# Kernel tuning notes

Measured on AMD Instinct MI355X. Metric: run time of the kernel, lower is better.

Reference implementation:

```python
import jax, jax.numpy as jnp
import numpy as np

B, L, E, H, K = 128, 512, 512, 256, 64


def setup_inputs() -> dict:
    key = jax.random.key(0)
    ks = jax.random.split(key, 13)
    s = 1.0 / np.sqrt(H)

    def u(k, shape):
        return jax.random.uniform(k, shape, jnp.float32, -s, s)

    return {
        "input_batch": jax.random.normal(ks[0], (B, L, E), jnp.float32),
        "labels": jax.random.randint(ks[1], (B, L), 0, K),
        "w_ih_f": u(ks[2], (4 * H, E)),
        "w_hh_f": u(ks[3], (4 * H, H)),
        "b_ih_f": u(ks[4], (4 * H,)),
        "b_hh_f": u(ks[5], (4 * H,)),
        "w_ih_b": u(ks[6], (4 * H, E)),
        "w_hh_b": u(ks[7], (4 * H, H)),
        "b_ih_b": u(ks[8], (4 * H,)),
        "b_hh_b": u(ks[9], (4 * H,)),
        "w_emit": u(ks[10], (K, 2 * H)),
        "b_emit": jnp.zeros((K,), jnp.float32),
        "transition": jax.random.normal(ks[11], (K, K), jnp.float32),
    }


def _lstm_dir(x, w_ih, w_hh, b_ih, b_hh):
    """One LSTM direction. x: (L,B,E) -> hidden states (L,B,H). PyTorch gate order i,f,g,o."""
    Hh = w_hh.shape[1]
    # input contribution for all timesteps at once: (L,B,4H)
    pre = jnp.einsum('lbe,ge->lbg', x, w_ih) + b_ih + b_hh

    def step(carry, p_t):
        h, c = carry
        g = p_t + h @ w_hh.T  # (B,4H)
        i, f, gg, o = jnp.split(g, 4, axis=-1)
        c = jax.nn.sigmoid(f) * c + jax.nn.sigmoid(i) * jnp.tanh(gg)
        h = jax.nn.sigmoid(o) * jnp.tanh(c)
        return (h, c), h

    init = (jnp.zeros((x.shape[1], Hh), x.dtype), jnp.zeros((x.shape[1], Hh), x.dtype))
    _, hs = jax.lax.scan(step, init, pre)
    return hs


def _bilstm_crf_loss(input_batch, labels, w_ih_f, w_hh_f, b_ih_f, b_hh_f,
                     w_ih_b, w_hh_b, b_ih_b, b_hh_b, w_emit, b_emit, transition):
    x = jnp.transpose(input_batch, (1, 0, 2))  # (L,B,E)
    h_f = _lstm_dir(x, w_ih_f, w_hh_f, b_ih_f, b_hh_f)
    h_b = _lstm_dir(x[::-1], w_ih_b, w_hh_b, b_ih_b, b_hh_b)[::-1]
    h = jnp.concatenate([h_f, h_b], axis=-1)  # (L,B,2H)
    emit = jnp.einsum('lbh,kh->b018'.replace('018', 'lk'), h, w_emit) + b_emit  # placeholder fixed below
    emit = jnp.einsum('lbh,kh->lbk', h, w_emit) + b_emit  # (L,B,K)
    emit = jnp.transpose(emit, (1, 0, 2))  # (B,L,K)

    # gold path score
    gold_emit = jnp.take_along_axis(emit, labels[:, :, None], axis=2)[:, :, 0]  # (B,L)
    gold_trans = transition[labels[:, :-1], labels[:, 1:]]  # (B,L-1)
    total_score = gold_emit.sum(axis=1) + gold_trans.sum(axis=1)  # (B,)

    # CRF forward algorithm (log partition), scan over timesteps 1..L-1
    def crf_step(d, e_t):
        # d: (B,K) log alpha; e_t: (B,K) emit at step t
        d = jax.nn.logsumexp(d[:, :, None] + transition[None, :, :] + e_t[:, None, :], axis=1)
        return d, None

    d0 = emit[:, 0]  # (B,K)
    dT, _ = jax.lax.scan(crf_step, d0, jnp.transpose(emit[:, 1:], (1, 0, 2)))
    log_z = jax.nn.logsumexp(dT, axis=1)  # (B,)
    return -(total_score - log_z)  # (B,)


def reference(input_batch, labels, w_ih_f, w_hh_f, b_ih_f, b_hh_f,
              w_ih_b, w_hh_b, b_ih_b, b_hh_b, w_emit, b_emit, transition):
    return _bilstm_crf_loss(input_batch, labels, w_ih_f, w_hh_f, b_ih_f, b_hh_f,
                            w_ih_b, w_hh_b, b_ih_b, b_hh_b, w_emit, b_emit, transition)
```

## Files before the change

### kernel.cpp

```cpp
#include <hip/hip_runtime.h>
#include <hip/hip_bf16.h>

#define B_   128
#define L_   512
#define E_   512
#define H_   256
#define K_   64
#define G4H  1024
#define LOG2E 1.4426950408889634f

typedef __bf16 bf16x8 __attribute__((ext_vector_type(8)));
typedef float  f32x4  __attribute__((ext_vector_type(4)));
typedef int    i32x8  __attribute__((ext_vector_type(8)));

__device__ inline unsigned short f2bf(float f) {
    unsigned int x = __builtin_bit_cast(unsigned int, f);
    unsigned int r = (x + 0x7fffu + ((x >> 16) & 1u)) >> 16;
    return (unsigned short)r;
}
__device__ inline float bf2f(unsigned short u) {
    unsigned int x = ((unsigned int)u) << 16;
    return __builtin_bit_cast(float, x);
}
__device__ inline unsigned int pack2(float lo, float hi) {
    return (unsigned int)f2bf(lo) | ((unsigned int)f2bf(hi) << 16);
}
__device__ inline float ex2(float x) { return __builtin_amdgcn_exp2f(x); }
__device__ inline float rcp_(float x) { return __builtin_amdgcn_rcpf(x); }

__device__ inline void gl_lds16(const unsigned short* g, unsigned short* l) {
    __builtin_amdgcn_global_load_lds(
        (const __attribute__((address_space(1))) unsigned int*)g,
        (__attribute__((address_space(3))) unsigned int*)l, 16, 0, 0);
}

__global__ void setup_convert(const float* __restrict__ whh_f, const float* __restrict__ whh_b,
                              const float* __restrict__ wemit,
                              const float* __restrict__ wihf, const float* __restrict__ wihb,
                              const float* __restrict__ bihf, const float* __restrict__ bhhf,
                              const float* __restrict__ bihb, const float* __restrict__ bhhb,
                              unsigned char* __restrict__ whh8,
                              unsigned short* __restrict__ wemit_bf,
                              unsigned short* __restrict__ wp,
                              float* __restrict__ bias_p) {
    int i = blockIdx.x * 256 + threadIdx.x;
    if (i < 262144) {
        int j = 2 * i;
        float v0 = (j < 262144) ? whh_f[j] : whh_b[j - 262144];
        float v1 = (j + 1 < 262144) ? whh_f[j + 1] : whh_b[j + 1 - 262144];
        int pk = __builtin_amdgcn_cvt_pk_fp8_f32(v0 * LOG2E, v1 * LOG2E, 0, false);
        ((unsigned short*)whh8)[i] = (unsigned short)(pk & 0xffff);
    }
    if (i < K_ * 2 * H_) wemit_bf[i] = f2bf(wemit[i]);
    if (i < 131072) {
        int rp = i >> 6;
        int k8 = (i & 63) * 8;
        int dd = rp >> 10, np = rp & 1023;
        int srow = (np & 3) * 256 + (np >> 2);
        const float* src = (dd == 0 ? wihf : wihb) + (size_t)srow * 512 + k8;
        float4 a  = *reinterpret_cast<const float4*>(src);
        float4 b2 = *reinterpret_cast<const float4*>(src + 4);
        uint4 pk = { pack2(a.x * LOG2E, a.y * LOG2E), pack2(a.z * LOG2E, a.w * LOG2E),
                     pack2(b2.x * LOG2E, b2.y * LOG2E), pack2(b2.z * LOG2E, b2.w * LOG2E) };
        *reinterpret_cast<uint4*>(wp + (size_t)rp * 512 + k8) = pk;
    }
    if (i < 2048) {
        int dd = i >> 10, np = i & 1023;
        int srow = (np & 3) * 256 + (np >> 2);
        bias_p[i] = ((dd == 0) ? (bihf[srow] + bhhf[srow]) : (bihb[srow] + bhhb[srow])) * LOG2E;
    }
}

__global__ void convert_x(const float* __restrict__ x, unsigned short* __restrict__ xb) {
    int i = blockIdx.x * 256 + threadIdx.x;
    float4 a = reinterpret_cast<const float4*>(x)[i * 2];
    float4 b = reinterpret_cast<const float4*>(x)[i * 2 + 1];
    uint4 p = { pack2(a.x, a.y), pack2(a.z, a.w), pack2(b.x, b.y), pack2(b.z, b.w) };
    reinterpret_cast<uint4*>(xb)[i] = p;
}

__global__ __launch_bounds__(256) void pre_gemm(
    const unsigned short* __restrict__ xb,
    const unsigned short* __restrict__ wp,
    const float* __restrict__ bias_p,
    unsigned short* __restrict__ pre3)
{
    __shared__ unsigned short A_lds[128 * 32];
    __shared__ unsigned short B_lds[128 * 32];

    int nt = blockIdx.x, mt = blockIdx.y;
    int tid = threadIdx.x;
    int n0 = nt * 128;
    int b  = mt >> 2, l0 = (mt & 3) * 128;
    int w = tid >> 6, lane = tid & 63;
    int q = lane >> 4, ln = lane & 15;
    int wm = (w >> 1) * 64, wn = (w & 1) * 64;

    f32x4 acc[4][4];
    #pragma unroll
    for (int i = 0; i < 4; ++i)
        #pragma unroll
        for (int j = 0; j < 4; ++j) acc[i][j] = (f32x4){0.f, 0.f, 0.f, 0.f};

    int r_ = tid >> 2, kp = (tid & 3) * 8;
    const unsigned short* asrc0 = xb + ((size_t)b * 512 + l0 + r_) * 512 + kp;
    const unsigned short* asrc1 = asrc0 + (size_t)64 * 512;
    const unsigned short* bsrc0 = wp + (size_t)(n0 + r_) * 512 + kp;
    const unsigned short* bsrc1 = bsrc0 + (size_t)64 * 512;
    unsigned short* adst0 = &A_lds[tid * 8];
    unsigned short* adst1 = &A_lds[2048 + tid * 8];
    unsigned short* bdst0 = &B_lds[tid * 8];
    unsigned short* bdst1 = &B_lds[2048 + tid * 8];

    for (int kc = 0; kc < 16; ++kc) {
        int k0 = kc * 32;
        gl_lds16(asrc0 + k0, adst0);
        gl_lds16(asrc1 + k0, adst1);
        gl_lds16(bsrc0 + k0, bdst0);
        gl_lds16(bsrc1 + k0, bdst1);
        __syncthreads();

        bf16x8 af[4], bfv[4];
        #pragma unroll
        for (int ms = 0; ms < 4; ++ms)
            af[ms] = *reinterpret_cast<const bf16x8*>(&A_lds[(wm + ms * 16 + ln) * 32 + q * 8]);
        #pragma unroll
        for (int ns = 0; ns < 4; ++ns)
            bfv[ns] = *reinterpret_cast<const bf16x8*>(&B_lds[(wn + ns * 16 + ln) * 32 + q * 8]);
        #pragma unroll
        for (int ms = 0; ms < 4; ++ms)
            #pragma unroll
            for (int ns = 0; ns < 4; ++ns)
                acc[ms][ns] = __builtin_amdgcn_mfma_f32_16x16x32_bf16(af[ms], bfv[ns], acc[ms][ns], 0, 0, 0);
        __syncthreads();
    }

    #pragma unroll
    for (int ns = 0; ns < 4; ++ns) {
        int n = n0 + wn + ns * 16 + ln;
        float bias = bias_p[n];
        int dsel = n >> 10, np = n & 1023;
        #pragma unroll
        for (int ms = 0; ms < 4; ++ms) {
            #pragma unroll
            for (int rg = 0; rg < 4; ++rg) {
                int l = l0 + wm + ms * 16 + q * 4 + rg;
                pre3[(((size_t)dsel * 128 + b) * 512 + l) * 1024 + np] = f2bf(acc[ms][ns][rg] + bias);
            }
        }
    }
}

__global__ __launch_bounds__(512, 2) void lstm_scan(
    const unsigned short* __restrict__ pre3,
    const unsigned char* __restrict__ whh8,
    unsigned short* __restrict__ hcat)
{
    __shared__ unsigned char h_lds[2][256];

    int wg = blockIdx.x;
    int d = wg >> 7, b = wg & 127;
    int tid = threadIdx.x, w = tid >> 6, lane = tid & 63;
    int q = lane >> 4, ln = lane & 15;

    const unsigned char* whh_d = whh8 + (size_t)d * (1024 * 256);
    const unsigned short* pre_wg = pre3 + ((size_t)d * 128 + b) * (512 * 1024);

    i32x8 wh[4][2][2];
    #pragma unroll
    for (int g = 0; g < 4; ++g)
        #pragma unroll
        for (int s = 0; s < 2; ++s) {
            int row = g * 256 + (w + 8 * s) * 16 + ln;
            #pragma unroll
            for (int kc = 0; kc < 2; ++kc)
                wh[g][s][kc] = *reinterpret_cast<const i32x8*>(
                    whh_d + (size_t)row * 256 + kc * 128 + q * 32);
        }

    if (tid < 128) ((int*)h_lds)[tid] = 0;

    bool act = (lane < 32);
    int s_  = (lane >> 4) & 1;
    int col = (w + 8 * s_) * 16 + ln;

    ushort4 p0 = {0,0,0,0}, p1 = {0,0,0,0};
    if (act) {
        int la  = (d == 0) ? 0 : (L_ - 1);
        int lb_ = (d == 0) ? 1 : (L_ - 2);
        p0 = *reinterpret_cast<const ushort4*>(pre_wg + (size_t)la * 1024 + col * 4);
        p1 = *reinterpret_cast<const ushort4*>(pre_wg + (size_t)lb_ * 1024 + col * 4);
    }
    __syncthreads();

    float cst = 0.f;

    for (int t = 0; t < L_; ++t) {
        int p = t & 1;
        int l = (d == 0) ? t : (L_ - 1 - t);

        ushort4 p2 = {0,0,0,0};
        if (act) {
            int t2 = (t + 2 < L_) ? (t + 2) : (L_ - 1);
            int l2 = (d == 0) ? t2 : (L_ - 1 - t2);
            p2 = *reinterpret_cast<const ushort4*>(pre_wg + (size_t)l2 * 1024 + col * 4);
        }

        const unsigned char* hb = h_lds[p];
        uint4 a00 = *reinterpret_cast<const uint4*>(hb + q * 32);
        uint4 a01 = *reinterpret_cast<const uint4*>(hb + q * 32 + 16);
        uint4 a10 = *reinterpret_cast<const uint4*>(hb + 128 + q * 32);
        uint4 a11 = *reinterpret_cast<const uint4*>(hb + 128 + q * 32 + 16);
        i32x8 af0 = { (int)a00.x, (int)a00.y, (int)a00.z, (int)a00.w,
                      (int)a01.x, (int)a01.y, (int)a01.z, (int)a01.w };
        i32x8 af1 = { (int)a10.x, (int)a10.y, (int)a10.z, (int)a10.w,
                      (int)a11.x, (int)a11.y, (int)a11.z, (int)a11.w };

        f32x4 acc[4][2];
        #pragma unroll
        for (int g = 0; g < 4; ++g) {
            acc[g][0] = (f32x4){0.f, 0.f, 0.f, 0.f};
            acc[g][1] = (f32x4){0.f, 0.f, 0.f, 0.f};
        }
        #pragma unroll
        for (int g = 0; g < 4; ++g)
            acc[g][0] = __builtin_amdgcn_mfma_scale_f32_16x16x128_f8f6f4(
                af0, wh[g][0][0], acc[g][0], 0, 0, 0, 0x7f7f7f7f, 0, 0x7f7f7f7f);
        #pragma unroll
        for (int g = 0; g < 4; ++g)
            acc[g][0] = __builtin_amdgcn_mfma_scale_f32_16x16x128_f8f6f4(
                af1, wh[g][0][1], acc[g][0], 0, 0, 0, 0x7f7f7f7f, 0, 0x7f7f7f7f);
        float lo[4];
        #pragma unroll
        for (int g = 0; g < 4; ++g) lo[g] = __shfl(acc[g][0][0], ln);
        __builtin_amdgcn_sched_barrier(0);
        #pragma unroll
        for (int g = 0; g < 4; ++g)
            acc[g][1] = __builtin_amdgcn_mfma_scale_f32_16x16x128_f8f6f4(
                af0, wh[g][1][0], acc[g][1], 0, 0, 0, 0x7f7f7f7f, 0, 0x7f7f7f7f);
        #pragma unroll
        for (int g = 0; g < 4; ++g)
            acc[g][1] = __builtin_amdgcn_mfma_scale_f32_16x16x128_f8f6f4(
                af1, wh[g][1][1], acc[g][1], 0, 0, 0, 0x7f7f7f7f, 0, 0x7f7f7f7f);
        float hi[4];
        #pragma unroll
        for (int g = 0; g < 4; ++g) hi[g] = __shfl(acc[g][1][0], ln);

        if (act) {
            float vi = (s_ ? hi[0] : lo[0]) + bf2f(p0.x);
            float vf = (s_ ? hi[1] : lo[1]) + bf2f(p0.y);
            float vg = (s_ ? hi[2] : lo[2]) + bf2f(p0.z);
            float vo = (s_ ? hi[3] : lo[3]) + bf2f(p0.w);
            float ei  = ex2(vi);
            float e2g = ex2(vg + vg);
            float itg = (ei * (e2g - 1.f)) * rcp_((1.f + ei) * (1.f + e2g));
            float sf  = rcp_(1.f + ex2(-vf));
            float cn  = fmaf(sf, cst, itg);
            cst = cn;
            float tc  = fmaf(-2.f, rcp_(1.f + ex2((2.f * LOG2E) * cn)), 1.f);
            float so  = rcp_(1.f + ex2(-vo));
            float hn  = so * tc;
            int pk = __builtin_amdgcn_cvt_pk_fp8_f32(hn, hn, 0, false);
            h_lds[p ^ 1][col] = (unsigned char)(pk & 0xff);
            hcat[((size_t)l * 128 + b) * 512 + d * 256 + col] = f2bf(hn);
        }
        __syncthreads();

        p0 = p1; p1 = p2;
    }
}

__global__ __launch_bounds__(256) void emit_gemm(
    const unsigned short* __restrict__ hcat,
    const unsigned short* __restrict__ wemit,
    const float* __restrict__ bemit,
    float* __restrict__ emit)
{
    int m0 = blockIdx.x * 64;
    int tid = threadIdx.x, w = tid >> 6, lane = tid & 63;
    int quad = lane >> 4, ln = lane & 15;
    int mrow = m0 + w * 16;

    f32x4 acc[4];
    #pragma unroll
    for (int i = 0; i < 4; ++i) acc[i] = (f32x4){0.f, 0.f, 0.f, 0.f};

    const unsigned short* arow = hcat + (size_t)(mrow + ln) * 512;
    #pragma unroll 4
    for (int kc = 0; kc < 16; ++kc) {
        bf16x8 af = *reinterpret_cast<const bf16x8*>(arow + kc * 32 + quad * 8);
        #pragma unroll
        for (int T = 0; T < 4; ++T) {
            bf16x8 bfv = *reinterpret_cast<const bf16x8*>(wemit + (size_t)(T * 16 + ln) * 512 + kc * 32 + quad * 8);
            acc[T] = __builtin_amdgcn_mfma_f32_16x16x32_bf16(af, bfv, acc[T], 0, 0, 0);
        }
    }
    #pragma unroll
    for (int T = 0; T < 4; ++T) {
        int k = T * 16 + ln;
        float bias = bemit[k];
        #pragma unroll
        for (int rg = 0; rg < 4; ++rg) {
            int m = mrow + quad * 4 + rg;
            int ll = m >> 7, bidx = m & 127;
            emit[((size_t)bidx * L_ + ll) * K_ + k] = acc[T][rg] + bias;
        }
    }
}

__global__ __launch_bounds__(64) void crf_kernel(
    const float* __restrict__ emit,
    const int* __restrict__ labels,
    const float* __restrict__ trans,
    float* __restrict__ out)
{
    __shared__ float els[2][64];
    int b = blockIdx.x, lane = threadIdx.x;
    const float* eb = emit + (size_t)b * L_ * K_;
    const int* lb = labels + (size_t)b * L_;

    float gold = 0.f;
    for (int t = lane; t < L_; t += 64) gold += eb[(size_t)t * K_ + lb[t]];
    for (int t = lane; t < L_ - 1; t += 64) gold += trans[lb[t] * K_ + lb[t + 1]];
    #pragma unroll
    for (int off = 32; off; off >>= 1) gold += __shfl_down(gold, off);

    float expT[64];
    #pragma unroll
    for (int i = 0; i < 64; ++i) expT[i] = __expf(trans[i * K_ + lane]);

    float dstate = eb[lane];
    float enext = eb[K_ + lane];
    for (int t = 1; t < L_; ++t) {
        float ecur = enext;
        if (t + 1 < L_) enext = eb[(size_t)(t + 1) * K_ + lane];
        float M = __builtin_amdgcn_readfirstlane(dstate);
        float e = __expf(dstate - M);
        float* el = els[t & 1];
        el[lane] = e;
        asm volatile("s_waitcnt lgkmcnt(0)" ::: "memory");
        float s0 = 0.f, s1 = 0.f, s2 = 0.f, s3 = 0.f;
        #pragma unroll
        for (int i = 0; i < 64; i += 16) {
            float4 a0 = *reinterpret_cast<const float4*>(&el[i]);
            float4 a1 = *reinterpret_cast<const float4*>(&el[i + 4]);
            float4 a2 = *reinterpret_cast<const float4*>(&el[i + 8]);
            float4 a3 = *reinterpret_cast<const float4*>(&el[i + 12]);
            s0 = fmaf(a0.x, expT[i], s0);      s0 = fmaf(a0.y, expT[i + 1], s0);
            s0 = fmaf(a0.z, expT[i + 2], s0);  s0 = fmaf(a0.w, expT[i + 3], s0);
            s1 = fmaf(a1.x, expT[i + 4], s1);  s1 = fmaf(a1.y, expT[i + 5], s1);
            s1 = fmaf(a1.z, expT[i + 6], s1);  s1 = fmaf(a1.w, expT[i + 7], s1);
            s2 = fmaf(a2.x, expT[i + 8], s2);  s2 = fmaf(a2.y, expT[i + 9], s2);
            s2 = fmaf(a2.z, expT[i + 10], s2); s2 = fmaf(a2.w, expT[i + 11], s2);
            s3 = fmaf(a3.x, expT[i + 12], s3); s3 = fmaf(a3.y, expT[i + 13], s3);
            s3 = fmaf(a3.z, expT[i + 14], s3); s3 = fmaf(a3.w, expT[i + 15], s3);
        }
        dstate = M + __logf((s0 + s1) + (s2 + s3)) + ecur;
    }
    float M = __builtin_amdgcn_readfirstlane(dstate);
    float e = __expf(dstate - M);
    float s = e;
    #pragma unroll
    for (int off = 32; off; off >>= 1) s += __shfl_xor(s, off);
    float logZ = M + __logf(s);
    if (lane == 0) out[b] = -(gold - logZ);
}

#define OFF_PRE    ((size_t)0)
#define OFF_EMIT   OFF_PRE
#define OFF_HCAT   ((size_t)268435456)
#define OFF_XB     OFF_HCAT
#define OFF_WHH8   ((size_t)(OFF_HCAT + 67108864))
#define OFF_WEMIT  ((size_t)(OFF_WHH8 + 524288))
#define OFF_WP     ((size_t)(OFF_WEMIT + 65536))
#define OFF_BIAS   ((size_t)(OFF_WP + 2097152))

extern "C" void kernel_launch(void* const* d_in, const int* in_sizes, int n_in,
                              void* d_out, int out_size, void* d_ws, size_t ws_size,
                              hipStream_t stream) {
    const float* x      = (const float*)d_in[0];
    const int*   labels = (const int*)d_in[1];
    const float* wihf   = (const float*)d_in[2];
    const float* whhf   = (const float*)d_in[3];
    const float* bihf   = (const float*)d_in[4];
    const float* bhhf   = (const float*)d_in[5];
    const float* wihb   = (const float*)d_in[6];
    const float* whhb   = (const float*)d_in[7];
    const float* bihb   = (const float*)d_in[8];
    const float* bhhb   = (const float*)d_in[9];
    const float* wemit  = (const float*)d_in[10];
    const float* bemit  = (const float*)d_in[11];
    const float* trans  = (const float*)d_in[12];
    float* out = (float*)d_out;

    char* ws = (char*)d_ws;
    unsigned short* pre3   = (unsigned short*)(ws + OFF_PRE);
    unsigned short* hcat   = (unsigned short*)(ws + OFF_HCAT);
    unsigned short* xb     = (unsigned short*)(ws + OFF_XB);
    float*          emit   = (float*)(ws + OFF_EMIT);
    unsigned char*  whh8   = (unsigned char*)(ws + OFF_WHH8);
    unsigned short* we_bf  = (unsigned short*)(ws + OFF_WEMIT);
    unsigned short* wp     = (unsigned short*)(ws + OFF_WP);
    float*          bias_p = (float*)(ws + OFF_BIAS);

    setup_convert<<<1024, 256, 0, stream>>>(whhf, whhb, wemit, wihf, wihb,
                                            bihf, bhhf, bihb, bhhb,
                                            whh8, we_bf, wp, bias_p);
    convert_x<<<16384, 256, 0, stream>>>(x, xb);
    pre_gemm<<<dim3(16, 512), 256, 0, stream>>>(xb, wp, bias_p, pre3);
    lstm_scan<<<256, 512, 0, stream>>>(pre3, whh8, hcat);
    emit_gemm<<<1024, 256, 0, stream>>>(hcat, we_bf, bemit, emit);
    crf_kernel<<<128, 64, 0, stream>>>(emit, labels, trans, out);
}
```

Baseline: 1.107 ms.

## Skew LSTM recurrence halves across two barriers to overlap MFMA with gate math

Splits each recurrent timestep into two phases, each closed by a barrier. Lanes handling the lower half of the hidden columns finish their gates in phase two of step t. Lanes handling the upper half finish theirs for step t-1 in phase one of step t, while the first-half K-chunk MFMAs are issuing. This software-pipelines the dependency chain so gate math overlaps matrix work. In exchange it adds a second barrier per step, a prologue and epilogue, and more complex indexing that must keep the h buffers consistent.

```diff
diff --git a/kernel.cpp b/kernel.cpp
--- a/kernel.cpp
+++ b/kernel.cpp
@@ -186,71 +186,49 @@
 
     ushort4 p0 = {0,0,0,0}, p1 = {0,0,0,0};
     if (act) {
-        int la  = (d == 0) ? 0 : (L_ - 1);
-        int lb_ = (d == 0) ? 1 : (L_ - 2);
-        p0 = *reinterpret_cast<const ushort4*>(pre_wg + (size_t)la * 1024 + col * 4);
-        p1 = *reinterpret_cast<const ushort4*>(pre_wg + (size_t)lb_ * 1024 + col * 4);
+        int ta = 0;
+        int tb = 1 - s_;
+        int la  = (d == 0) ? ta : (L_ - 1 - ta);
+        int lb2 = (d == 0) ? tb : (L_ - 1 - tb);
+        p0 = *reinterpret_cast<const ushort4*>(pre_wg + (size_t)la  * 1024 + col * 4);
+        p1 = *reinterpret_cast<const ushort4*>(pre_wg + (size_t)lb2 * 1024 + col * 4);
     }
     __syncthreads();
 
     float cst = 0.f;
+    float hic[4] = {0.f, 0.f, 0.f, 0.f};
 
     for (int t = 0; t < L_; ++t) {
-        int p = t & 1;
-        int l = (d == 0) ? t : (L_ - 1 - t);
-
-        ushort4 p2 = {0,0,0,0};
+        int rb = t & 1;
+
+        ushort4 p2v = {0,0,0,0};
         if (act) {
-            int t2 = (t + 2 < L_) ? (t + 2) : (L_ - 1);
+            int t2 = t + 2 - s_;
+            if (t2 > L_ - 1) t2 = L_ - 1;
             int l2 = (d == 0) ? t2 : (L_ - 1 - t2);
-            p2 = *reinterpret_cast<const ushort4*>(pre_wg + (size_t)l2 * 1024 + col * 4);
-        }
-
-        const unsigned char* hb = h_lds[p];
+            p2v = *reinterpret_cast<const ushort4*>(pre_wg + (size_t)l2 * 1024 + col * 4);
+        }
+
+        const unsigned char* hb = h_lds[rb];
         uint4 a00 = *reinterpret_cast<const uint4*>(hb + q * 32);
         uint4 a01 = *reinterpret_cast<const uint4*>(hb + q * 32 + 16);
-        uint4 a10 = *reinterpret_cast<const uint4*>(hb + 128 + q * 32);
-        uint4 a11 = *reinterpret_cast<const uint4*>(hb + 128 + q * 32 + 16);
         i32x8 af0 = { (int)a00.x, (int)a00.y, (int)a00.z, (int)a00.w,
                       (int)a01.x, (int)a01.y, (int)a01.z, (int)a01.w };
-        i32x8 af1 = { (int)a10.x, (int)a10.y, (int)a10.z, (int)a10.w,
-                      (int)a11.x, (int)a11.y, (int)a11.z, (int)a11.w };
-
+        f32x4 z4 = (f32x4){0.f, 0.f, 0.f, 0.f};
         f32x4 acc[4][2];
         #pragma unroll
         for (int g = 0; g < 4; ++g) {
-            acc[g][0] = (f32x4){0.f, 0.f, 0.f, 0.f};
-            acc[g][1] = (f32x4){0.f, 0.f, 0.f, 0.f};
-        }
-        #pragma unroll
-        for (int g = 0; g < 4; ++g)
             acc[g][0] = __builtin_amdgcn_mfma_scale_f32_16x16x128_f8f6f4(
-                af0, wh[g][0][0], acc[g][0], 0, 0, 0, 0x7f7f7f7f, 0, 0x7f7f7f7f);
-        #pragma unroll
-        for (int g = 0; g < 4; ++g)
-            acc[g][0] = __builtin_amdgcn_mfma_scale_f32_16x16x128_f8f6f4(
-                af1, wh[g][0][1], acc[g][0], 0, 0, 0, 0x7f7f7f7f, 0, 0x7f7f7f7f);
-        float lo[4];
-        #pragma unroll
-        for (int g = 0; g < 4; ++g) lo[g] = __shfl(acc[g][0][0], ln);
-        __builtin_amdgcn_sched_barrier(0);
-        #pragma unroll
-        for (int g = 0; g < 4; ++g)
+                af0, wh[g][0][0], z4, 0, 0, 0, 0x7f7f7f7f, 0, 0x7f7f7f7f);
             acc[g][1] = __builtin_amdgcn_mfma_scale_f32_16x16x128_f8f6f4(
-                af0, wh[g][1][0], acc[g][1], 0, 0, 0, 0x7f7f7f7f, 0, 0x7f7f7f7f);
-        #pragma unroll
-        for (int g = 0; g < 4; ++g)
-            acc[g][1] = __builtin_amdgcn_mfma_scale_f32_16x16x128_f8f6f4(
-                af1, wh[g][1][1], acc[g][1], 0, 0, 0, 0x7f7f7f7f, 0, 0x7f7f7f7f);
-        float hi[4];
-        #pragma unroll
-        for (int g = 0; g < 4; ++g) hi[g] = __shfl(acc[g][1][0], ln);
-
-        if (act) {
-            float vi = (s_ ? hi[0] : lo[0]) + bf2f(p0.x);
-            float vf = (s_ ? hi[1] : lo[1]) + bf2f(p0.y);
-            float vg = (s_ ? hi[2] : lo[2]) + bf2f(p0.z);
-            float vo = (s_ ? hi[3] : lo[3]) + bf2f(p0.w);
+                af0, wh[g][1][0], z4, 0, 0, 0, 0x7f7f7f7f, 0, 0x7f7f7f7f);
+        }
+
+        if (act && s_ && t > 0) {
+            float vi = hic[0] + bf2f(p0.x);
+            float vf = hic[1] + bf2f(p0.y);
+            float vg = hic[2] + bf2f(p0.z);
+            float vo = hic[3] + bf2f(p0.w);
             float ei  = ex2(vi);
             float e2g = ex2(vg + vg);
             float itg = (ei * (e2g - 1.f)) * rcp_((1.f + ei) * (1.f + e2g));
@@ -261,12 +239,70 @@
             float so  = rcp_(1.f + ex2(-vo));
             float hn  = so * tc;
             int pk = __builtin_amdgcn_cvt_pk_fp8_f32(hn, hn, 0, false);
-            h_lds[p ^ 1][col] = (unsigned char)(pk & 0xff);
+            h_lds[rb][col] = (unsigned char)(pk & 0xff);
+            int l = (d == 0) ? (t - 1) : (L_ - t);
             hcat[((size_t)l * 128 + b) * 512 + d * 256 + col] = f2bf(hn);
         }
-        __syncthreads();
-
-        p0 = p1; p1 = p2;
+        asm volatile("s_waitcnt lgkmcnt(0)" ::: "memory");
+        __builtin_amdgcn_s_barrier();
+
+        uint4 a10 = *reinterpret_cast<const uint4*>(hb + 128 + q * 32);
+        uint4 a11 = *reinterpret_cast<const uint4*>(hb + 128 + q * 32 + 16);
+        i32x8 af1 = { (int)a10.x, (int)a10.y, (int)a10.z, (int)a10.w,
+                      (int)a11.x, (int)a11.y, (int)a11.z, (int)a11.w };
+        #pragma unroll
+        for (int g = 0; g < 4; ++g)
+            acc[g][0] = __builtin_amdgcn_mfma_scale_f32_16x16x128_f8f6f4(
+                af1, wh[g][0][1], acc[g][0], 0, 0, 0, 0x7f7f7f7f, 0, 0x7f7f7f7f);
+        #pragma unroll
+        for (int g = 0; g < 4; ++g)
+            acc[g][1] = __builtin_amdgcn_mfma_scale_f32_16x16x128_f8f6f4(
+                af1, wh[g][1][1], acc[g][1], 0, 0, 0, 0x7f7f7f7f, 0, 0x7f7f7f7f);
+
+        if (act && !s_) {
+            float vi = acc[0][0][0] + bf2f(p0.x);
+            float vf = acc[1][0][0] + bf2f(p0.y);
+            float vg = acc[2][0][0] + bf2f(p0.z);
+            float vo = acc[3][0][0] + bf2f(p0.w);
+            float ei  = ex2(vi);
+            float e2g = ex2(vg + vg);
+            float itg = (ei * (e2g - 1.f)) * rcp_((1.f + ei) * (1.f + e2g));
+            float sf  = rcp_(1.f + ex2(-vf));
+            float cn  = fmaf(sf, cst, itg);
+            cst = cn;
+            float tc  = fmaf(-2.f, rcp_(1.f + ex2((2.f * LOG2E) * cn)), 1.f);
+            float so  = rcp_(1.f + ex2(-vo));
+            float hn  = so * tc;
+            int pk = __builtin_amdgcn_cvt_pk_fp8_f32(hn, hn, 0, false);
+            h_lds[rb ^ 1][col] = (unsigned char)(pk & 0xff);
+            int l = (d == 0) ? t : (L_ - 1 - t);
+            hcat[((size_t)l * 128 + b) * 512 + d * 256 + col] = f2bf(hn);
+        }
+
+        #pragma unroll
+        for (int g = 0; g < 4; ++g) hic[g] = __shfl(acc[g][1][0], ln);
+
+        asm volatile("s_waitcnt lgkmcnt(0)" ::: "memory");
+        __builtin_amdgcn_s_barrier();
+
+        p0 = p1; p1 = p2v;
+    }
+
+    if (act && s_) {
+        float vi = hic[0] + bf2f(p0.x);
+        float vf = hic[1] + bf2f(p0.y);
+        float vg = hic[2] + bf2f(p0.z);
+        float vo = hic[3] + bf2f(p0.w);
+        float ei  = ex2(vi);
+        float e2g = ex2(vg + vg);
+        float itg = (ei * (e2g - 1.f)) * rcp_((1.f + ei) * (1.f + e2g));
+        float sf  = rcp_(1.f + ex2(-vf));
+        float cn  = fmaf(sf, cst, itg);
+        float tc  = fmaf(-2.f, rcp_(1.f + ex2((2.f * LOG2E) * cn)), 1.f);
+        float so  = rcp_(1.f + ex2(-vo));
+        float hn  = so * tc;
+        int l = (d == 0) ? (L_ - 1) : 0;
+        hcat[((size_t)l * 128 + b) * 512 + d * 256 + col] = f2bf(hn);
     }
 }
 
```

Result: slower. 1.165 ms (+5.3%).
